# Optimization experiments

Hardware: AMD Instinct MI355X
Metric: run time of the kernel (lower is better)

Reference implementation:

```python
import jax, jax.numpy as jnp
import numpy as np

W, H = 256, 256          # image width (x) and height (y); image indexed [x, y] like the torch code
N = 8192                 # depth-sorted visible gaussians
TILE = 16                # tile_size default
CHUNK = 128              # gaussians composited per scan step (N % CHUNK == 0)
MIN_WEIGHT = 1e-6        # early-termination threshold from render_pixel


def setup_inputs() -> dict:
    key = jax.random.key(0)
    k1, k2, k3, k4, k5 = jax.random.split(key, 5)
    # pixel-space means, uniformly over the image
    points_xy = jax.random.uniform(k1, (N, 2), dtype=jnp.float32) * jnp.array([W, H], jnp.float32)
    # SPD inverse 2D covariances: Sigma = R diag(var) R^T, inv = R diag(1/var) R^T
    theta = jax.random.uniform(k2, (N,), dtype=jnp.float32) * (2.0 * np.pi)
    sig = jax.random.uniform(k3, (N, 2), dtype=jnp.float32, minval=1.5, maxval=8.0)
    var = sig ** 2
    ct, st = jnp.cos(theta), jnp.sin(theta)
    R = jnp.stack([jnp.stack([ct, -st], -1), jnp.stack([st, ct], -1)], -2)  # [N,2,2]
    inverse_covariance = jnp.einsum('nij,nj,nkj->nik', R, 1.0 / var, R)
    # radius = ceil(2.5 * sqrt(max eigenvalue)) as in compute_radius
    radius = jnp.ceil(2.5 * jnp.sqrt(jnp.max(var, axis=1)))
    colors = jax.random.uniform(k4, (N, 3), dtype=jnp.float32)
    opacity = jax.random.normal(k5, (N,), dtype=jnp.float32)  # pre-sigmoid logits
    return dict(points_xy=points_xy, inverse_covariance=inverse_covariance,
                radius=radius, colors=colors, opacity=opacity)


def _rasterize(points_xy, inverse_covariance, radius, colors, opacity):
    px = jnp.arange(W, dtype=jnp.float32)[:, None]   # [W,1] pixel x coords
    py = jnp.arange(H, dtype=jnp.float32)[None, :]   # [1,H] pixel y coords
    # tile origin for each pixel (tile-based culling as in render_image)
    tile_x0 = ((jnp.arange(W) // TILE) * TILE).astype(jnp.float32)[:, None]  # [W,1]
    tile_y0 = ((jnp.arange(H) // TILE) * TILE).astype(jnp.float32)[None, :]  # [1,H]
    # per-gaussian bounding boxes (preprocess)
    min_x = jnp.floor(points_xy[:, 0] - radius); max_x = jnp.ceil(points_xy[:, 0] + radius)
    min_y = jnp.floor(points_xy[:, 1] - radius); max_y = jnp.ceil(points_xy[:, 1] + radius)

    n_chunks = N // CHUNK
    def chunk(a):
        return a.reshape((n_chunks, CHUNK) + a.shape[1:])
    xs = dict(mx=chunk(points_xy[:, 0]), my=chunk(points_xy[:, 1]),
              a=chunk(inverse_covariance[:, 0, 0]), b=chunk(inverse_covariance[:, 0, 1]),
              c=chunk(inverse_covariance[:, 1, 1]),
              mnx=chunk(min_x), mxx=chunk(max_x), mny=chunk(min_y), mxy=chunk(max_y),
              col=chunk(colors), op=chunk(opacity))

    @jax.checkpoint
    def body(carry, ch):
        T, color = carry  # T: [W,H] remaining transmittance; color: [W,H,3]
        dx = px[None] - ch['mx'][:, None, None]  # [C,W,1]
        dy = py[None] - ch['my'][:, None, None]  # [C,1,H]
        # mahalanobis form d^T Sigma^{-1} d with symmetric inv cov [[a,b],[b,c]]
        q = (ch['a'][:, None, None] * dx * dx
             + 2.0 * ch['b'][:, None, None] * dx * dy
             + ch['c'][:, None, None] * dy * dy)              # [C,W,H]
        alpha = jnp.exp(-0.5 * q) * jax.nn.sigmoid(ch['op'])[:, None, None]
        # gaussian participates for a pixel iff its bbox intersects that pixel's tile
        in_tile = ((ch['mnx'][:, None, None] <= tile_x0[None] + TILE)
                   & (ch['mxx'][:, None, None] >= tile_x0[None])
                   & (ch['mny'][:, None, None] <= tile_y0[None] + TILE)
                   & (ch['mxy'][:, None, None] >= tile_y0[None]))   # [C,W,H]
        alpha = jnp.where(in_tile, alpha, 0.0)
        cum = jnp.cumprod(1.0 - alpha, axis=0)                 # inclusive prefix of (1-alpha)
        T_before = T[None] * jnp.concatenate([jnp.ones_like(cum[:1]), cum[:-1]], axis=0)
        # original: test_weight = T_before*(1-alpha); terminate (skip contribution) if < min_weight
        include = (T[None] * cum) >= MIN_WEIGHT
        contrib = jnp.where(include, T_before * alpha, 0.0)   # [C,W,H]
        color = color + jnp.einsum('cwh,cd->whd', contrib, ch['col'])
        return (T * cum[-1], color), None

    init = (jnp.ones((W, H), jnp.float32), jnp.zeros((W, H, 3), jnp.float32))
    (_, color), _ = jax.lax.scan(body, init, xs)
    return color  # [W,H,3] image indexed [x,y]


def reference(points_xy, inverse_covariance, radius, colors, opacity):
    return _rasterize(points_xy, inverse_covariance, radius, colors, opacity)
```

## Files before the change

kernel.cpp:

```cpp
#include <hip/hip_runtime.h>
#include <hip/hip_fp16.h>

#define WIDTH   256
#define HEIGHT  256
#define NG      8192
#define TILE_SZ 16
#define MINW    1e-6f
#define BLK     1024
#define NBATCH  (NG / BLK)
#define NWAVE   (BLK / 64)
#define NSEG    16
#define PXB     128
#define RSZ     1024

__global__ __launch_bounds__(BLK, 8) void raster_kernel(
    const float* __restrict__ pts,
    const float* __restrict__ icov,
    const float* __restrict__ rad,
    const float* __restrict__ cols,
    const float* __restrict__ opac,
    float* __restrict__ out)
{
    __shared__ unsigned long long s_ball[NBATCH * NWAVE];
    __shared__ int s_pfx[NBATCH * NWAVE];
    __shared__ unsigned short s_list[NG];
    __shared__ float4 s_g[RSZ * 2];
    __shared__ float s_P[NSEG][PXB];
    float* s_red = (float*)s_g;

    const int tid  = threadIdx.x;
    const int lane = tid & 63;
    const int wave = tid >> 6;
    const int seg  = tid >> 6;
    const int pair = tid & 63;
    const float tx0 = (float)(blockIdx.x * TILE_SZ);
    const float ty0 = (float)(blockIdx.y * TILE_SZ);
    const float tx1 = tx0 + (float)TILE_SZ;
    const float ty1 = ty0 + (float)TILE_SZ;

    unsigned int hitbits = 0;
    for (int b = 0; b < NBATCH; ++b) {
        const int g = b * BLK + tid;
        const float2 p = ((const float2*)pts)[g];
        const float  r = rad[g];
        bool hit = (floorf(p.x - r) <= tx1) & (ceilf(p.x + r) >= tx0)
                 & (floorf(p.y - r) <= ty1) & (ceilf(p.y + r) >= ty0);
        unsigned long long m = __ballot(hit);
        if (lane == 0) s_ball[b * NWAVE + wave] = m;
        if (hit) hitbits |= (1u << b);
    }
    __syncthreads();
    if (wave == 0) {
        int v0 = __popcll(s_ball[lane]);
        int v1 = __popcll(s_ball[64 + lane]);
        #pragma unroll
        for (int d = 1; d < 64; d <<= 1) {
            const int t0 = __shfl_up(v0, d);
            const int t1 = __shfl_up(v1, d);
            if (lane >= d) { v0 += t0; v1 += t1; }
        }
        s_pfx[lane] = v0;
        s_pfx[64 + lane] = v1 + __shfl(v0, 63);
    }
    __syncthreads();
    const int count = s_pfx[127];
    {
        unsigned int hb = hitbits;
        const unsigned long long ltmask = (1ull << lane) - 1ull;
        while (hb) {
            const int b = __ffs(hb) - 1;  hb &= hb - 1;
            const int idx = b * NWAVE + wave;
            const unsigned long long m = s_ball[idx];
            const int bs = idx ? s_pfx[idx - 1] : 0;
            s_list[bs + __popcll(m & ltmask)] = (unsigned short)(b * BLK + tid);
        }
    }
    __syncthreads();

    const int pA = pair;
    const int pB = pair + 64;
    const float fy  = ty0 + (float)(pair & 15);
    const float fxA = tx0 + (float)(blockIdx.z * 8 + (pair >> 4));
    const float fxB = fxA + 4.0f;
    const float kc = -0.72134752044f;
    float TA = 1.0f, TB = 1.0f;
    float arA = 0.f, agA = 0.f, abA = 0.f, arB = 0.f, agB = 0.f, abB = 0.f;

    for (int base = 0; base < count; base += RSZ) {
        const int n = min(RSZ, count - base);
        if (tid < n) {
            const int g = s_list[base + tid];
            const float2 p = ((const float2*)pts)[g];
            const float4 ic = ((const float4*)icov)[g];
            const float op = 1.0f / (1.0f + __expf(-opac[g]));
            const __half2 h = __floats2half2_rn(cols[3 * g], cols[3 * g + 1]);
            unsigned rgbits; __builtin_memcpy(&rgbits, &h, 4);
            s_g[tid * 2 + 0] = make_float4(p.x, p.y, kc * ic.x, 2.0f * kc * ic.y);
            s_g[tid * 2 + 1] = make_float4(kc * ic.w, op, __uint_as_float(rgbits),
                                           cols[3 * g + 2]);
        }
        __syncthreads();

        const int L  = (n + NSEG - 1) >> 4;
        const int i0 = seg * L;
        const int i1 = min(i0 + L, n);

        float PA = 1.0f, PB = 1.0f;
        float lrA = 0.f, lgA = 0.f, lbA = 0.f, lrB = 0.f, lgB = 0.f, lbB = 0.f;
        if (__ballot((TA >= MINW) || (TB >= MINW)) != 0ull) {
            #pragma unroll 4
            for (int i = i0; i < i1; ++i) {
                const float4 g0 = s_g[i * 2 + 0];
                const float4 g1 = s_g[i * 2 + 1];
                const float dy    = fy - g0.y;
                const float bdy   = g0.w * dy;
                const float cdydy = (g1.x * dy) * dy;
                const unsigned rgbits = __float_as_uint(g1.z);
                __half2 h; __builtin_memcpy(&h, &rgbits, 4);
                const float2 rg = __half22float2(h);
                const float dxA = fxA - g0.x;
                const float qA  = fmaf(fmaf(g0.z, dxA, bdy), dxA, cdydy);
                const float aA  = g1.y * __builtin_amdgcn_exp2f(qA);
                const float wA  = PA * aA;
                lrA = fmaf(wA, rg.x, lrA);
                lgA = fmaf(wA, rg.y, lgA);
                lbA = fmaf(wA, g1.w, lbA);
                PA  = fmaf(-aA, PA, PA);
                const float dxB = fxB - g0.x;
                const float qB  = fmaf(fmaf(g0.z, dxB, bdy), dxB, cdydy);
                const float aB  = g1.y * __builtin_amdgcn_exp2f(qB);
                const float wB  = PB * aB;
                lrB = fmaf(wB, rg.x, lrB);
                lgB = fmaf(wB, rg.y, lgB);
                lbB = fmaf(wB, g1.w, lbB);
                PB  = fmaf(-aB, PB, PB);
            }
        }
        s_P[seg][pA] = PA;
        s_P[seg][pB] = PB;
        __syncthreads();

        float TinA = TA, TnxA = TA, TinB = TB, TnxB = TB;
        #pragma unroll
        for (int s = 0; s < NSEG; ++s) {
            const float vA = s_P[s][pA];
            const float vB = s_P[s][pB];
            if (s < seg) { TinA *= vA; TinB *= vB; }
            TnxA *= vA;  TnxB *= vB;
        }

        const bool aliveA = (TinA >= MINW), aliveB = (TinB >= MINW);
        const bool gatedA = aliveA && (TinA * PA < MINW);
        const bool gatedB = aliveB && (TinB * PB < MINW);
        if (aliveA && !gatedA) {
            arA = fmaf(TinA, lrA, arA); agA = fmaf(TinA, lgA, agA); abA = fmaf(TinA, lbA, abA);
        }
        if (aliveB && !gatedB) {
            arB = fmaf(TinB, lrB, arB); agB = fmaf(TinB, lgB, agB); abB = fmaf(TinB, lbB, abB);
        }
        if (__ballot(gatedA || gatedB) != 0ull) {
            float TlA = TinA, TlB = TinB;
            for (int i = i0; i < i1; ++i) {
                const float4 g0 = s_g[i * 2 + 0];
                const float4 g1 = s_g[i * 2 + 1];
                const float dy    = fy - g0.y;
                const float bdy   = g0.w * dy;
                const float cdydy = (g1.x * dy) * dy;
                const unsigned rgbits = __float_as_uint(g1.z);
                __half2 h; __builtin_memcpy(&h, &rgbits, 4);
                const float2 rg = __half22float2(h);
                const float dxA = fxA - g0.x;
                const float aA  = g1.y * __builtin_amdgcn_exp2f(
                                      fmaf(fmaf(g0.z, dxA, bdy), dxA, cdydy));
                const float TnA = TlA * (1.0f - aA);
                const float wA  = (gatedA && TnA >= MINW) ? TlA * aA : 0.0f;
                arA = fmaf(wA, rg.x, arA); agA = fmaf(wA, rg.y, agA); abA = fmaf(wA, g1.w, abA);
                TlA = TnA;
                const float dxB = fxB - g0.x;
                const float aB  = g1.y * __builtin_amdgcn_exp2f(
                                      fmaf(fmaf(g0.z, dxB, bdy), dxB, cdydy));
                const float TnB = TlB * (1.0f - aB);
                const float wB  = (gatedB && TnB >= MINW) ? TlB * aB : 0.0f;
                arB = fmaf(wB, rg.x, arB); agB = fmaf(wB, rg.y, agB); abB = fmaf(wB, g1.w, abB);
                TlB = TnB;
            }
        }
        TA = TnxA;  TB = TnxB;
        if (__syncthreads_count((TA < MINW) && (TB < MINW)) == BLK) break;
    }

    s_red[seg * (PXB * 3) + pA * 3 + 0] = arA;
    s_red[seg * (PXB * 3) + pA * 3 + 1] = agA;
    s_red[seg * (PXB * 3) + pA * 3 + 2] = abA;
    s_red[seg * (PXB * 3) + pB * 3 + 0] = arB;
    s_red[seg * (PXB * 3) + pB * 3 + 1] = agB;
    s_red[seg * (PXB * 3) + pB * 3 + 2] = abB;
    __syncthreads();
    if (tid < PXB * 3) {
        float v = 0.0f;
        #pragma unroll
        for (int s = 0; s < NSEG; ++s) v += s_red[s * (PXB * 3) + tid];
        const int p  = tid / 3;
        const int ch = tid - 3 * p;
        const int x = blockIdx.x * TILE_SZ + blockIdx.z * 8 + (p >> 4);
        const int y = blockIdx.y * TILE_SZ + (p & 15);
        out[(x * HEIGHT + y) * 3 + ch] = v;
    }
}

extern "C" void kernel_launch(void* const* d_in, const int* in_sizes, int n_in,
                              void* d_out, int out_size, void* d_ws, size_t ws_size,
                              hipStream_t stream) {
    const float* pts  = (const float*)d_in[0];
    const float* icov = (const float*)d_in[1];
    const float* rad  = (const float*)d_in[2];
    const float* cols = (const float*)d_in[3];
    const float* opac = (const float*)d_in[4];
    float* out = (float*)d_out;
    dim3 grid(WIDTH / TILE_SZ, HEIGHT / TILE_SZ, 2);
    raster_kernel<<<grid, dim3(BLK), 0, stream>>>(pts, icov, rad, cols, opac, out);
}
```

Before: 83.05 us.

## Precompute gaussian table in prep kernel and cover whole tile per block

Adds a prep kernel that computes each gaussian's packed parameters (scaled inverse covariance, sigmoid opacity, half-packed colors) once into a workspace table. The raster kernel then just copies table entries into shared memory instead of recomputing them per tile. Each block now covers the full 16x16 tile rather than half of it, with 8 depth segments of 128 pixel-pairs and a 512-entry staging ring. This halves the grid and removes redundant culling and list building per tile, in exchange for less parallelism, an extra launch and a shared-memory pool aliased between the list, staging and reduction buffers.

```diff
diff --git a/kernel.cpp b/kernel.cpp
--- a/kernel.cpp
+++ b/kernel.cpp
@@ -9,30 +9,45 @@
 #define BLK     1024
 #define NBATCH  (NG / BLK)
 #define NWAVE   (BLK / 64)
-#define NSEG    16
-#define PXB     128
-#define RSZ     1024
-
-__global__ __launch_bounds__(BLK, 8) void raster_kernel(
+#define NSEG    8
+#define RSZ     512
+#define KC      (-0.72134752044f)
+
+__global__ __launch_bounds__(256) void prep_kernel(
+    const float* __restrict__ pts, const float* __restrict__ icov,
+    const float* __restrict__ cols, const float* __restrict__ opac,
+    float4* __restrict__ table)
+{
+    const int g = blockIdx.x * 256 + threadIdx.x;
+    const float2 p = ((const float2*)pts)[g];
+    const float4 ic = ((const float4*)icov)[g];
+    const float op = 1.0f / (1.0f + __expf(-opac[g]));
+    const __half2 h = __floats2half2_rn(cols[3 * g], cols[3 * g + 1]);
+    unsigned rgbits; __builtin_memcpy(&rgbits, &h, 4);
+    table[2 * g + 0] = make_float4(p.x, p.y, KC * ic.x, 2.0f * KC * ic.y);
+    table[2 * g + 1] = make_float4(KC * ic.w, op, __uint_as_float(rgbits),
+                                   cols[3 * g + 2]);
+}
+
+__global__ __launch_bounds__(BLK, 4) void raster_kernel(
     const float* __restrict__ pts,
-    const float* __restrict__ icov,
     const float* __restrict__ rad,
-    const float* __restrict__ cols,
-    const float* __restrict__ opac,
+    const float4* __restrict__ table,
     float* __restrict__ out)
 {
     __shared__ unsigned long long s_ball[NBATCH * NWAVE];
     __shared__ int s_pfx[NBATCH * NWAVE];
-    __shared__ unsigned short s_list[NG];
-    __shared__ float4 s_g[RSZ * 2];
-    __shared__ float s_P[NSEG][PXB];
-    float* s_red = (float*)s_g;
+    __shared__ __align__(16) char s_pool[32768];
+    unsigned short* s_list = (unsigned short*)s_pool;
+    float4* s_g = (float4*)(s_pool + 16384);
+    float*  s_red = (float*)s_pool;
+    __shared__ float s_P[NSEG][256];
 
     const int tid  = threadIdx.x;
     const int lane = tid & 63;
     const int wave = tid >> 6;
-    const int seg  = tid >> 6;
-    const int pair = tid & 63;
+    const int seg  = tid >> 7;
+    const int pair = tid & 127;
     const float tx0 = (float)(blockIdx.x * TILE_SZ);
     const float ty0 = (float)(blockIdx.y * TILE_SZ);
     const float tx1 = tx0 + (float)TILE_SZ;
@@ -77,12 +92,10 @@
     }
     __syncthreads();
 
-    const int pA = pair;
-    const int pB = pair + 64;
+    const int pA = pair, pB = pair + 128;
     const float fy  = ty0 + (float)(pair & 15);
-    const float fxA = tx0 + (float)(blockIdx.z * 8 + (pair >> 4));
-    const float fxB = fxA + 4.0f;
-    const float kc = -0.72134752044f;
+    const float fxA = tx0 + (float)(pair >> 4);
+    const float fxB = fxA + 8.0f;
     float TA = 1.0f, TB = 1.0f;
     float arA = 0.f, agA = 0.f, abA = 0.f, arB = 0.f, agB = 0.f, abB = 0.f;
 
@@ -90,18 +103,12 @@
         const int n = min(RSZ, count - base);
         if (tid < n) {
             const int g = s_list[base + tid];
-            const float2 p = ((const float2*)pts)[g];
-            const float4 ic = ((const float4*)icov)[g];
-            const float op = 1.0f / (1.0f + __expf(-opac[g]));
-            const __half2 h = __floats2half2_rn(cols[3 * g], cols[3 * g + 1]);
-            unsigned rgbits; __builtin_memcpy(&rgbits, &h, 4);
-            s_g[tid * 2 + 0] = make_float4(p.x, p.y, kc * ic.x, 2.0f * kc * ic.y);
-            s_g[tid * 2 + 1] = make_float4(kc * ic.w, op, __uint_as_float(rgbits),
-                                           cols[3 * g + 2]);
+            s_g[tid * 2 + 0] = table[2 * g + 0];
+            s_g[tid * 2 + 1] = table[2 * g + 1];
         }
         __syncthreads();
 
-        const int L  = (n + NSEG - 1) >> 4;
+        const int L  = (n + NSEG - 1) >> 3;
         const int i0 = seg * L;
         const int i1 = min(i0 + L, n);
 
@@ -189,20 +196,20 @@
         if (__syncthreads_count((TA < MINW) && (TB < MINW)) == BLK) break;
     }
 
-    s_red[seg * (PXB * 3) + pA * 3 + 0] = arA;
-    s_red[seg * (PXB * 3) + pA * 3 + 1] = agA;
-    s_red[seg * (PXB * 3) + pA * 3 + 2] = abA;
-    s_red[seg * (PXB * 3) + pB * 3 + 0] = arB;
-    s_red[seg * (PXB * 3) + pB * 3 + 1] = agB;
-    s_red[seg * (PXB * 3) + pB * 3 + 2] = abB;
-    __syncthreads();
-    if (tid < PXB * 3) {
+    s_red[(seg * 256 + pA) * 3 + 0] = arA;
+    s_red[(seg * 256 + pA) * 3 + 1] = agA;
+    s_red[(seg * 256 + pA) * 3 + 2] = abA;
+    s_red[(seg * 256 + pB) * 3 + 0] = arB;
+    s_red[(seg * 256 + pB) * 3 + 1] = agB;
+    s_red[(seg * 256 + pB) * 3 + 2] = abB;
+    __syncthreads();
+    if (tid < 256 * 3) {
         float v = 0.0f;
         #pragma unroll
-        for (int s = 0; s < NSEG; ++s) v += s_red[s * (PXB * 3) + tid];
+        for (int s = 0; s < NSEG; ++s) v += s_red[s * 768 + tid];
         const int p  = tid / 3;
         const int ch = tid - 3 * p;
-        const int x = blockIdx.x * TILE_SZ + blockIdx.z * 8 + (p >> 4);
+        const int x = blockIdx.x * TILE_SZ + (p >> 4);
         const int y = blockIdx.y * TILE_SZ + (p & 15);
         out[(x * HEIGHT + y) * 3 + ch] = v;
     }
@@ -217,6 +224,8 @@
     const float* cols = (const float*)d_in[3];
     const float* opac = (const float*)d_in[4];
     float* out = (float*)d_out;
-    dim3 grid(WIDTH / TILE_SZ, HEIGHT / TILE_SZ, 2);
-    raster_kernel<<<grid, dim3(BLK), 0, stream>>>(pts, icov, rad, cols, opac, out);
+    float4* table = (float4*)d_ws;
+    prep_kernel<<<NG / 256, 256, 0, stream>>>(pts, icov, cols, opac, table);
+    dim3 grid(WIDTH / TILE_SZ, HEIGHT / TILE_SZ);
+    raster_kernel<<<grid, dim3(BLK), 0, stream>>>(pts, rad, table, out);
 }
```

After: 81.91 us. About the same (-1.4%).
